# Performance work log

Measured on AMD Instinct MI355X. Metric: run time of the kernel, lower is better.

## Reference

```python
import jax, jax.numpy as jnp
import numpy as np

B, N, M, C, H = 2, 256, 512, 256, 8
Dh = C // H          # head dim = 32
F = 256              # frequency_embedding_size
MAX_PERIOD = 10000.0


def setup_inputs() -> dict:
    rng = jax.random.key(0)
    ks = jax.random.split(rng, 12)
    s = 0.02

    def w(k, shape):
        return jax.random.normal(k, shape, jnp.float32) * s

    inp = {
        "query": jax.random.normal(ks[0], (B, N, C), jnp.float32),
        "key": jax.random.normal(ks[1], (B, M, C), jnp.float32),
        "query_pos": jax.random.uniform(ks[2], (B, N, M), jnp.float32),
        # attention projections (torch Linear stores W as (out,in))
        "Wq": w(ks[3], (C, C)), "bq": jnp.zeros((C,), jnp.float32),
        "Wk": w(ks[4], (C, C)),
        "Wv": w(ks[5], (C, C)), "bv": jnp.zeros((C,), jnp.float32),
        "Wo": w(ks[6], (C, C)), "bo": jnp.zeros((C,), jnp.float32),
        # ScalarEmbedder MLP: Linear(F, C) -> SiLU -> Linear(C, C)
        "W1": w(ks[7], (C, F)), "b1": jnp.zeros((C,), jnp.float32),
        "W2": w(ks[8], (C, C)), "b2": jnp.zeros((C,), jnp.float32),
        "freqs": jnp.exp(-np.log(MAX_PERIOD) * jnp.arange(F // 2, dtype=jnp.float32) / (F // 2)),
    }
    return inp


def reference(query, key, query_pos, Wq, bq, Wk, Wv, bv, Wo, bo, W1, b1, W2, b2, freqs):
    scale = Dh ** (-0.5)
    # projections -> (B, H, N/M, Dh)
    q = (query @ Wq.T + bq).reshape(B, N, H, Dh).transpose(0, 2, 1, 3)
    k = (key @ Wk.T).reshape(B, M, H, Dh).transpose(0, 2, 1, 3)
    v = (key @ Wv.T + bv).reshape(B, M, H, Dh).transpose(0, 2, 1, 3)
    # scalar positional embedding per (n, m) pair
    t = query_pos.reshape(-1)                              # (B*N*M,)
    tf = t[:, None] * freqs                                # (B*N*M, F/2)
    emb = jnp.concatenate([jnp.cos(tf), jnp.sin(tf)], -1)  # (B*N*M, F)
    pe = jax.nn.silu(emb @ W1.T + b1) @ W2.T + b2          # (B*N*M, C)
    pe = pe.reshape(B, N, M, H, Dh).transpose(0, 3, 1, 2, 4)  # (B,H,N,M,Dh)
    # gated scores: (q[:,:,:,None] * pe) . k  ==  einsum over d
    attn = jnp.einsum('bhnd,bhnmd,bhmd->bhnm', q, pe, k) * scale
    attn = jax.nn.softmax(attn, axis=-1)
    x = jnp.einsum('bhnm,bhmd->bhnd', attn, v)             # (B,H,N,Dh)
    x = x.transpose(0, 2, 1, 3).reshape(B, N, C)
    return x @ Wo.T + bo + query
```

## Files before the change

### kernel.cpp

```cpp
#include <hip/hip_runtime.h>

#define Bn 2
#define Nn 256
#define Mn 512
#define Cn 256
#define Hn 8
#define MT 64
#define SCALE_ 0.17677669529663687f

typedef short bf16x8 __attribute__((ext_vector_type(8)));
typedef short bf16x4 __attribute__((ext_vector_type(4)));
typedef float f32x4 __attribute__((ext_vector_type(4)));

static __device__ __forceinline__ float b2f(short s) {
    unsigned u = ((unsigned)(unsigned short)s) << 16;
    return __builtin_bit_cast(float, u);
}
static __device__ __forceinline__ short f2b(float f) {
    unsigned u = __builtin_bit_cast(unsigned, f);
    u += 0x7fffu + ((u >> 16) & 1u);
    return (short)(u >> 16);
}
static __device__ __forceinline__ void async16(const void* g, void* l) {
    __builtin_amdgcn_global_load_lds(
        (const __attribute__((address_space(1))) unsigned int*)g,
        (__attribute__((address_space(3))) unsigned int*)l, 16, 0, 0);
}
static __device__ __forceinline__ int taddr(int c, int mm) {
    return (c >> 3) * 1040 + (c & 7) * 128 + (((mm >> 3) ^ (c & 7)) << 4) + (mm & 7) * 2;
}

__global__ __launch_bounds__(256) void prep(
        const float* __restrict__ query, const float* __restrict__ key,
        const float* __restrict__ Wq, const float* __restrict__ bq,
        const float* __restrict__ Wk, const float* __restrict__ Wv,
        const float* __restrict__ bv, const float* __restrict__ W1,
        const float* __restrict__ W2, short* __restrict__ W1b,
        short* __restrict__ W2b, float* __restrict__ qp,
        short* __restrict__ kTb, short* __restrict__ vTb) {
    __shared__ float arow[32][Cn];
    const int bid = blockIdx.x;
    const int t = threadIdx.x;
    if (bid < 256) {
        const int i = bid * 256 + t;
        W1b[i] = f2b(W1[i]);
        W2b[i] = f2b(W2[i]);
        return;
    }
    int task, id;
    if (bid < 320)      { task = 0; id = bid - 256; }
    else if (bid < 448) { task = 1; id = bid - 320; }
    else                { task = 2; id = bid - 448; }
    const int r0 = (id >> 2) * 32;
    const int c0 = (id & 3) * 64;
    const float* A = (task == 0) ? query : key;
    const float* W = (task == 0) ? Wq : (task == 1 ? Wk : Wv);
    #pragma unroll
    for (int i = 0; i < 32; ++i) arow[i][t] = A[(size_t)(r0 + i) * Cn + t];
    __syncthreads();
    const int col = c0 + (t & 63);
    const int rg = (t >> 6) * 8;
    float acc[8];
    #pragma unroll
    for (int i = 0; i < 8; ++i) acc[i] = 0.f;
    const float* wr = W + (size_t)col * Cn;
    for (int k = 0; k < Cn; k += 4) {
        const float4 wv = *(const float4*)(wr + k);
        #pragma unroll
        for (int i = 0; i < 8; ++i)
            acc[i] += arow[rg + i][k] * wv.x + arow[rg + i][k+1] * wv.y
                    + arow[rg + i][k+2] * wv.z + arow[rg + i][k+3] * wv.w;
    }
    if (task == 0) {
        const float bvv = bq[col];
        #pragma unroll
        for (int i = 0; i < 8; ++i)
            qp[(size_t)(r0 + rg + i) * Cn + col] = acc[i] + bvv;
    } else {
        const float bvv = (task == 2) ? bv[col] : 0.f;
        short* outb = (task == 2) ? vTb : kTb;
        const int b = r0 >> 9, mloc = (r0 & 511) + rg;
        bf16x8 p;
        #pragma unroll
        for (int i = 0; i < 8; ++i) p[i] = f2b(acc[i] + bvv);
        *(bf16x8*)(outb + ((size_t)(b * Cn + col)) * Mn + mloc) = p;
    }
}

__global__ __launch_bounds__(512)
__attribute__((amdgpu_waves_per_eu(2, 2)))
void fused_attn(
        const float* __restrict__ qp, const short* __restrict__ kTb,
        const short* __restrict__ vTb, const float* __restrict__ qpos,
        const short* __restrict__ W1b, const short* __restrict__ W2b,
        const float* __restrict__ b1, const float* __restrict__ b2,
        const float* __restrict__ freqs, float* __restrict__ xout) {
    __shared__ __align__(16) char embS[MT * 512];
    __shared__ __align__(16) char kTs[32 * 1040];
    __shared__ __align__(16) char vTs[32 * 1040];
    __shared__ float tposS[Mn];
    __shared__ float scb2[Hn * MT];
    __shared__ float pacc[512];
    __shared__ float corrS[Hn], lS[Hn];

    const int t = threadIdx.x;
    const int lane = t & 63;
    const int w = t >> 6;
    const int lr = lane & 15, lg = lane >> 4;

    const int qrow = ((blockIdx.x & 7) << 6) | (blockIdx.x >> 3);
    const int b = qrow >> 8;

    bf16x8 w1r[16], w2r[16];
    #pragma unroll
    for (int jb = 0; jb < 2; ++jb) {
        const short* p1 = W1b + (size_t)(w * 32 + jb * 16 + lr) * Cn + lg * 8;
        const short* p2 = W2b + (size_t)(w * 32 + jb * 16 + lr) * Cn + lg * 8;
        #pragma unroll
        for (int kk = 0; kk < 8; ++kk) {
            w1r[jb * 8 + kk] = *(const bf16x8*)(p1 + kk * 32);
            w2r[jb * 8 + kk] = *(const bf16x8*)(p2 + kk * 32);
        }
    }
    #pragma unroll
    for (int i = 0; i < 16; ++i) {
        asm volatile("" : "+v"(w1r[i]));
        asm volatile("" : "+v"(w2r[i]));
    }

    const int cA = w * 32 + lr, cB = cA + 16;
    const float b1v0 = b1[cA], b1v1 = b1[cB];
    const float b2v0 = b2[cA], b2v1 = b2[cB];
    const float q0 = qp[(size_t)qrow * Cn + cA];
    const float q1 = qp[(size_t)qrow * Cn + cB];
    const int fg = t & 7;
    float fr[16];
    #pragma unroll
    for (int j = 0; j < 16; ++j) fr[j] = freqs[fg * 16 + j];
    tposS[t] = qpos[(size_t)qrow * Mn + t];
    float m_run = -1e30f, l_run = 0.f;
    float xacc = 0.f;
    const f32x4 vzero = {0.f, 0.f, 0.f, 0.f};
    const int st_c = lane >> 3;
    const int st_ch = (lane & 7) ^ st_c;
    __syncthreads();

    for (int m0 = 0; m0 < Mn; m0 += MT) {
        {
            const size_t gb = (size_t)b * Cn * Mn + m0 + st_ch * 8;
            #pragma unroll
            for (int i = 0; i < 4; ++i) {
                const int seg = i * 8 + w;
                const size_t srow = gb + (size_t)(seg * 8 + st_c) * Mn;
                async16(kTb + srow, kTs + seg * 1040);
                async16(vTb + srow, vTs + seg * 1040);
            }
        }

        {
            const int m = t >> 3;
            const float tv = tposS[m0 + m];
            bf16x8 pc[2], ps[2];
            #pragma unroll
            for (int j = 0; j < 16; ++j) {
                float sv, cv;
                __sincosf(tv * fr[j], &sv, &cv);
                pc[j >> 3][j & 7] = f2b(cv);
                ps[j >> 3][j & 7] = f2b(sv);
            }
            char* rowp = embS + m * 512;
            const int sw = (m & 7) << 4;
            *(bf16x8*)(rowp + ((fg * 32) ^ sw)) = pc[0];
            *(bf16x8*)(rowp + ((fg * 32 + 16) ^ sw)) = pc[1];
            *(bf16x8*)(rowp + ((256 + fg * 32) ^ sw)) = ps[0];
            *(bf16x8*)(rowp + ((256 + fg * 32 + 16) ^ sw)) = ps[1];
        }
        __syncthreads();

        f32x4 acc[4][2];
        #pragma unroll
        for (int pb = 0; pb < 4; ++pb) { acc[pb][0] = vzero; acc[pb][1] = vzero; }
        #pragma unroll
        for (int pb = 0; pb < 4; ++pb) {
            const int row = pb * 16 + lr;
            const int sw = (row & 7) << 4;
            const char* rowp = embS + row * 512;
            #pragma unroll
            for (int kk = 0; kk < 8; ++kk) {
                const bf16x8 a = *(const bf16x8*)(rowp + ((lg * 16 + kk * 64) ^ sw));
                acc[pb][0] = __builtin_amdgcn_mfma_f32_16x16x32_bf16(a, w1r[kk],     acc[pb][0], 0, 0, 0);
                acc[pb][1] = __builtin_amdgcn_mfma_f32_16x16x32_bf16(a, w1r[8 + kk], acc[pb][1], 0, 0, 0);
            }
        }
        __syncthreads();

        #pragma unroll
        for (int pb = 0; pb < 4; ++pb) {
            #pragma unroll
            for (int jb = 0; jb < 2; ++jb) {
                const float bv = jb ? b1v1 : b1v0;
                const int j = w * 32 + jb * 16 + lr;
                #pragma unroll
                for (int r = 0; r < 4; ++r) {
                    const int row = pb * 16 + lg * 4 + r;
                    float hv = acc[pb][jb][r] + bv;
                    hv = hv / (1.f + __expf(-hv));
                    *(short*)(embS + row * 512 + ((j * 2) ^ ((row & 7) << 4))) = f2b(hv);
                }
            }
        }
        __syncthreads();

        #pragma unroll
        for (int pb = 0; pb < 4; ++pb) { acc[pb][0] = vzero; acc[pb][1] = vzero; }
        #pragma unroll
        for (int pb = 0; pb < 4; ++pb) {
            const int row = pb * 16 + lr;
            const int sw = (row & 7) << 4;
            const char* rowp = embS + row * 512;
            #pragma unroll
            for (int kk = 0; kk < 8; ++kk) {
                const bf16x8 a = *(const bf16x8*)(rowp + ((lg * 16 + kk * 64) ^ sw));
                acc[pb][0] = __builtin_amdgcn_mfma_f32_16x16x32_bf16(a, w2r[kk],     acc[pb][0], 0, 0, 0);
                acc[pb][1] = __builtin_amdgcn_mfma_f32_16x16x32_bf16(a, w2r[8 + kk], acc[pb][1], 0, 0, 0);
            }
        }

        #pragma unroll
        for (int pb = 0; pb < 4; ++pb) {
            const int mmb = pb * 16 + lg * 4;
            const bf16x4 k4a = *(const bf16x4*)(kTs + taddr(cA, mmb));
            const bf16x4 k4b = *(const bf16x4*)(kTs + taddr(cB, mmb));
            #pragma unroll
            for (int r = 0; r < 4; ++r) {
                float v = (acc[pb][0][r] + b2v0) * q0 * b2f(k4a[r])
                        + (acc[pb][1][r] + b2v1) * q1 * b2f(k4b[r]);
                v += __shfl_xor(v, 1);
                v += __shfl_xor(v, 2);
                v += __shfl_xor(v, 4);
                v += __shfl_xor(v, 8);
                if (lr == 0) scb2[w * MT + mmb + r] = v * SCALE_;
            }
        }

        {
            const float s = scb2[w * MT + lane];
            float tmax = s;
            #pragma unroll
            for (int msk = 1; msk < 64; msk <<= 1) tmax = fmaxf(tmax, __shfl_xor(tmax, msk));
            const float mnew = fmaxf(m_run, tmax);
            const float corr = __expf(m_run - mnew);
            const float e = __expf(s - mnew);
            scb2[w * MT + lane] = e;
            float ss = e;
            #pragma unroll
            for (int msk = 1; msk < 64; msk <<= 1) ss += __shfl_xor(ss, msk);
            l_run = l_run * corr + ss;
            m_run = mnew;
            if (lane == 0) corrS[w] = corr;
        }
        __syncthreads();

        {
            const int c = t & 255, half = t >> 8;
            const int h = c >> 5;
            const int rowb = (c >> 3) * 1040 + (c & 7) * 128;
            const int c7 = c & 7;
            const float* wr2 = scb2 + h * MT + half * 32;
            float s = 0.f;
            #pragma unroll
            for (int i = 0; i < 4; ++i) {
                const bf16x8 v8 = *(const bf16x8*)(vTs + rowb + (((half * 4 + i) ^ c7) << 4));
                const float4 wa = *(const float4*)(wr2 + i * 8);
                const float4 wb = *(const float4*)(wr2 + i * 8 + 4);
                s += wa.x * b2f(v8[0]) + wa.y * b2f(v8[1]) + wa.z * b2f(v8[2]) + wa.w * b2f(v8[3])
                   + wb.x * b2f(v8[4]) + wb.y * b2f(v8[5]) + wb.z * b2f(v8[6]) + wb.w * b2f(v8[7]);
            }
            pacc[t] = s;
        }
        __syncthreads();
        if (t < 256) xacc = xacc * corrS[t >> 5] + pacc[t] + pacc[t + 256];
    }

    if (lane == 0) lS[w] = l_run;
    __syncthreads();
    if (t < 256) xout[(size_t)qrow * Cn + t] = xacc / lS[t >> 5];
}

__global__ __launch_bounds__(256) void linear_out(
        const float* __restrict__ A, const float* __restrict__ W,
        const float* __restrict__ bias, const float* __restrict__ res,
        float* __restrict__ out) {
    __shared__ float arow[32][Cn];
    const int r0 = blockIdx.x * 32;
    const int c0 = blockIdx.y * 64;
    const int t = threadIdx.x;
    #pragma unroll
    for (int i = 0; i < 32; ++i) arow[i][t] = A[(size_t)(r0 + i) * Cn + t];
    __syncthreads();
    const int col = c0 + (t & 63);
    const int rg = (t >> 6) * 8;
    float acc[8];
    #pragma unroll
    for (int i = 0; i < 8; ++i) acc[i] = 0.f;
    const float* wr = W + (size_t)col * Cn;
    for (int k = 0; k < Cn; k += 4) {
        const float4 wv = *(const float4*)(wr + k);
        #pragma unroll
        for (int i = 0; i < 8; ++i)
            acc[i] += arow[rg + i][k] * wv.x + arow[rg + i][k+1] * wv.y
                    + arow[rg + i][k+2] * wv.z + arow[rg + i][k+3] * wv.w;
    }
    const float bvv = bias[col];
    #pragma unroll
    for (int i = 0; i < 8; ++i)
        out[(size_t)(r0 + rg + i) * Cn + col] =
            acc[i] + bvv + res[(size_t)(r0 + rg + i) * Cn + col];
}

extern "C" void kernel_launch(void* const* d_in, const int* in_sizes, int n_in,
                              void* d_out, int out_size, void* d_ws, size_t ws_size,
                              hipStream_t stream) {
    const float* query = (const float*)d_in[0];
    const float* key   = (const float*)d_in[1];
    const float* qpos  = (const float*)d_in[2];
    const float* Wq    = (const float*)d_in[3];
    const float* bq    = (const float*)d_in[4];
    const float* Wk    = (const float*)d_in[5];
    const float* Wv    = (const float*)d_in[6];
    const float* bv    = (const float*)d_in[7];
    const float* Wo    = (const float*)d_in[8];
    const float* bo    = (const float*)d_in[9];
    const float* W1    = (const float*)d_in[10];
    const float* b1    = (const float*)d_in[11];
    const float* W2    = (const float*)d_in[12];
    const float* b2    = (const float*)d_in[13];
    const float* freqs = (const float*)d_in[14];
    float* out = (float*)d_out;

    char* ws = (char*)d_ws;
    float* qp  = (float*)(ws);
    short* kTb = (short*)(ws + 524288);
    short* vTb = (short*)(ws + 1048576);
    float* xo  = (float*)(ws + 1572864);
    short* W1b = (short*)(ws + 2097152);
    short* W2b = (short*)(ws + 2228224);

    prep<<<576, 256, 0, stream>>>(query, key, Wq, bq, Wk, Wv, bv, W1, W2,
                                  W1b, W2b, qp, kTb, vTb);
    fused_attn<<<Bn * Nn, 512, 0, stream>>>(qp, kTb, vTb, qpos, W1b, W2b, b1, b2, freqs, xo);
    linear_out<<<dim3(16, 4), 256, 0, stream>>>(xo, Wo, bo, query, out);
}
```

Baseline: 299.8 us.

## Cut register and LDS use in fused attention, raise occupancy, re-grid projections

The fused attention kernel stops holding both W1 and W2 fragments in registers for the whole run. It keeps one shared register buffer and reloads W1 or W2 from global memory before each MLP stage. The async K/V staging into LDS is dropped, so K and V are read directly from global memory, and the launch bounds now request 4 blocks per CU. Sin/cos use hardware sinf/cosf on inputs pre-scaled by 1/2π. The prep and output-projection kernels are split into smaller tiles to launch more blocks. The trade-off is repeated weight and K/V global traffic and lower-precision trig in exchange for more waves in flight.

```diff
diff --git a/kernel.cpp b/kernel.cpp
--- a/kernel.cpp
+++ b/kernel.cpp
@@ -7,6 +7,7 @@
 #define Hn 8
 #define MT 64
 #define SCALE_ 0.17677669529663687f
+#define INV2PI 0.15915494309189535f
 
 typedef short bf16x8 __attribute__((ext_vector_type(8)));
 typedef short bf16x4 __attribute__((ext_vector_type(4)));
@@ -20,14 +21,6 @@
     unsigned u = __builtin_bit_cast(unsigned, f);
     u += 0x7fffu + ((u >> 16) & 1u);
     return (short)(u >> 16);
-}
-static __device__ __forceinline__ void async16(const void* g, void* l) {
-    __builtin_amdgcn_global_load_lds(
-        (const __attribute__((address_space(1))) unsigned int*)g,
-        (__attribute__((address_space(3))) unsigned int*)l, 16, 0, 0);
-}
-static __device__ __forceinline__ int taddr(int c, int mm) {
-    return (c >> 3) * 1040 + (c & 7) * 128 + (((mm >> 3) ^ (c & 7)) << 4) + (mm & 7) * 2;
 }
 
 __global__ __launch_bounds__(256) void prep(
@@ -47,58 +40,71 @@
         W2b[i] = f2b(W2[i]);
         return;
     }
-    int task, id;
-    if (bid < 320)      { task = 0; id = bid - 256; }
-    else if (bid < 448) { task = 1; id = bid - 320; }
-    else                { task = 2; id = bid - 448; }
-    const int r0 = (id >> 2) * 32;
-    const int c0 = (id & 3) * 64;
-    const float* A = (task == 0) ? query : key;
-    const float* W = (task == 0) ? Wq : (task == 1 ? Wk : Wv);
+    if (bid < 512) {
+        const int id = bid - 256;
+        const int r0 = (id >> 2) * 8, c0 = (id & 3) * 64;
+        #pragma unroll
+        for (int i = 0; i < 8; ++i)
+            if ((t >> 5) == i >> 2)
+                ;
+        #pragma unroll
+        for (int i = 0; i < 8; ++i) arow[i][t] = query[(size_t)(r0 + i) * Cn + t];
+        __syncthreads();
+        const int col = c0 + (t & 63);
+        const int rs = t >> 6;
+        float a0 = 0.f, a1 = 0.f;
+        const float* wr = Wq + (size_t)col * Cn;
+        for (int k = 0; k < Cn; k += 4) {
+            const float4 wv = *(const float4*)(wr + k);
+            const int r = rs * 2;
+            a0 += arow[r][k] * wv.x + arow[r][k+1] * wv.y
+                + arow[r][k+2] * wv.z + arow[r][k+3] * wv.w;
+            a1 += arow[r+1][k] * wv.x + arow[r+1][k+1] * wv.y
+                + arow[r+1][k+2] * wv.z + arow[r+1][k+3] * wv.w;
+        }
+        const float bvv = bq[col];
+        qp[(size_t)(r0 + rs * 2) * Cn + col] = a0 + bvv;
+        qp[(size_t)(r0 + rs * 2 + 1) * Cn + col] = a1 + bvv;
+        return;
+    }
+    const int isv = bid >= 768;
+    const int id = bid - (isv ? 768 : 512);
+    const int r0 = (id >> 3) * 32, c0 = (id & 7) * 32;
+    const float* W = isv ? Wv : Wk;
+    short* outb = isv ? vTb : kTb;
     #pragma unroll
-    for (int i = 0; i < 32; ++i) arow[i][t] = A[(size_t)(r0 + i) * Cn + t];
+    for (int i = 0; i < 32; ++i) arow[i][t] = key[(size_t)(r0 + i) * Cn + t];
     __syncthreads();
-    const int col = c0 + (t & 63);
-    const int rg = (t >> 6) * 8;
-    float acc[8];
-    #pragma unroll
-    for (int i = 0; i < 8; ++i) acc[i] = 0.f;
+    const int col = c0 + (t & 31);
+    const int rs = t >> 5;
+    float a4[4] = {0.f, 0.f, 0.f, 0.f};
     const float* wr = W + (size_t)col * Cn;
     for (int k = 0; k < Cn; k += 4) {
         const float4 wv = *(const float4*)(wr + k);
         #pragma unroll
-        for (int i = 0; i < 8; ++i)
-            acc[i] += arow[rg + i][k] * wv.x + arow[rg + i][k+1] * wv.y
-                    + arow[rg + i][k+2] * wv.z + arow[rg + i][k+3] * wv.w;
-    }
-    if (task == 0) {
-        const float bvv = bq[col];
-        #pragma unroll
-        for (int i = 0; i < 8; ++i)
-            qp[(size_t)(r0 + rg + i) * Cn + col] = acc[i] + bvv;
-    } else {
-        const float bvv = (task == 2) ? bv[col] : 0.f;
-        short* outb = (task == 2) ? vTb : kTb;
-        const int b = r0 >> 9, mloc = (r0 & 511) + rg;
-        bf16x8 p;
-        #pragma unroll
-        for (int i = 0; i < 8; ++i) p[i] = f2b(acc[i] + bvv);
-        *(bf16x8*)(outb + ((size_t)(b * Cn + col)) * Mn + mloc) = p;
-    }
-}
-
-__global__ __launch_bounds__(512)
-__attribute__((amdgpu_waves_per_eu(2, 2)))
-void fused_attn(
+        for (int i = 0; i < 4; ++i) {
+            const int r = rs * 4 + i;
+            a4[i] += arow[r][k] * wv.x + arow[r][k+1] * wv.y
+                   + arow[r][k+2] * wv.z + arow[r][k+3] * wv.w;
+        }
+    }
+    const float bvv = isv ? bv[col] : 0.f;
+    const int bk = r0 >> 9, mloc = (r0 & 511) + rs * 4;
+    bf16x4 p;
+    #pragma unroll
+    for (int i = 0; i < 4; ++i) p[i] = f2b(a4[i] + bvv);
+    *(bf16x4*)(outb + (size_t)(bk * Cn + col) * Mn + mloc) = p;
+}
+
+__global__ __launch_bounds__(512, 4) void fused_attn(
         const float* __restrict__ qp, const short* __restrict__ kTb,
         const short* __restrict__ vTb, const float* __restrict__ qpos,
         const short* __restrict__ W1b, const short* __restrict__ W2b,
         const float* __restrict__ b1, const float* __restrict__ b2,
         const float* __restrict__ freqs, float* __restrict__ xout) {
     __shared__ __align__(16) char embS[MT * 512];
-    __shared__ __align__(16) char kTs[32 * 1040];
-    __shared__ __align__(16) char vTs[32 * 1040];
     __shared__ float tposS[Mn];
+    __shared__ float fbuf[128];
     __shared__ float scb2[Hn * MT];
     __shared__ float pacc[512];
     __shared__ float corrS[Hn], lS[Hn];
@@ -111,62 +117,42 @@
     const int qrow = ((blockIdx.x & 7) << 6) | (blockIdx.x >> 3);
     const int b = qrow >> 8;
 
-    bf16x8 w1r[16], w2r[16];
+    const int cA = w * 32 + lr, cB = cA + 16;
+    const short* w1p0 = W1b + (size_t)cA * Cn + lg * 8;
+    const short* w1p1 = W1b + (size_t)cB * Cn + lg * 8;
+    const short* w2p0 = W2b + (size_t)cA * Cn + lg * 8;
+    const short* w2p1 = W2b + (size_t)cB * Cn + lg * 8;
+
+    bf16x8 wreg[16];
     #pragma unroll
-    for (int jb = 0; jb < 2; ++jb) {
-        const short* p1 = W1b + (size_t)(w * 32 + jb * 16 + lr) * Cn + lg * 8;
-        const short* p2 = W2b + (size_t)(w * 32 + jb * 16 + lr) * Cn + lg * 8;
-        #pragma unroll
-        for (int kk = 0; kk < 8; ++kk) {
-            w1r[jb * 8 + kk] = *(const bf16x8*)(p1 + kk * 32);
-            w2r[jb * 8 + kk] = *(const bf16x8*)(p2 + kk * 32);
-        }
-    }
-    #pragma unroll
-    for (int i = 0; i < 16; ++i) {
-        asm volatile("" : "+v"(w1r[i]));
-        asm volatile("" : "+v"(w2r[i]));
-    }
-
-    const int cA = w * 32 + lr, cB = cA + 16;
+    for (int kk = 0; kk < 8; ++kk) {
+        wreg[kk] = *(const bf16x8*)(w1p0 + kk * 32);
+        wreg[8 + kk] = *(const bf16x8*)(w1p1 + kk * 32);
+    }
+
     const float b1v0 = b1[cA], b1v1 = b1[cB];
     const float b2v0 = b2[cA], b2v1 = b2[cB];
     const float q0 = qp[(size_t)qrow * Cn + cA];
     const float q1 = qp[(size_t)qrow * Cn + cB];
-    const int fg = t & 7;
-    float fr[16];
-    #pragma unroll
-    for (int j = 0; j < 16; ++j) fr[j] = freqs[fg * 16 + j];
     tposS[t] = qpos[(size_t)qrow * Mn + t];
+    if (t < 128) fbuf[t] = freqs[t] * INV2PI;
+    const short* krow0 = kTb + (size_t)(b * Cn + cA) * Mn;
+    const short* krow1 = kTb + (size_t)(b * Cn + cB) * Mn;
     float m_run = -1e30f, l_run = 0.f;
     float xacc = 0.f;
     const f32x4 vzero = {0.f, 0.f, 0.f, 0.f};
-    const int st_c = lane >> 3;
-    const int st_ch = (lane & 7) ^ st_c;
     __syncthreads();
 
     for (int m0 = 0; m0 < Mn; m0 += MT) {
         {
-            const size_t gb = (size_t)b * Cn * Mn + m0 + st_ch * 8;
-            #pragma unroll
-            for (int i = 0; i < 4; ++i) {
-                const int seg = i * 8 + w;
-                const size_t srow = gb + (size_t)(seg * 8 + st_c) * Mn;
-                async16(kTb + srow, kTs + seg * 1040);
-                async16(vTb + srow, vTs + seg * 1040);
-            }
-        }
-
-        {
-            const int m = t >> 3;
+            const int m = t >> 3, fg = t & 7;
             const float tv = tposS[m0 + m];
             bf16x8 pc[2], ps[2];
             #pragma unroll
             for (int j = 0; j < 16; ++j) {
-                float sv, cv;
-                __sincosf(tv * fr[j], &sv, &cv);
-                pc[j >> 3][j & 7] = f2b(cv);
-                ps[j >> 3][j & 7] = f2b(sv);
+                const float xr = tv * fbuf[fg * 16 + j];
+                pc[j >> 3][j & 7] = f2b(__builtin_amdgcn_cosf(xr));
+                ps[j >> 3][j & 7] = f2b(__builtin_amdgcn_sinf(xr));
             }
             char* rowp = embS + m * 512;
             const int sw = (m & 7) << 4;
@@ -188,9 +174,14 @@
             #pragma unroll
             for (int kk = 0; kk < 8; ++kk) {
                 const bf16x8 a = *(const bf16x8*)(rowp + ((lg * 16 + kk * 64) ^ sw));
-                acc[pb][0] = __builtin_amdgcn_mfma_f32_16x16x32_bf16(a, w1r[kk],     acc[pb][0], 0, 0, 0);
-                acc[pb][1] = __builtin_amdgcn_mfma_f32_16x16x32_bf16(a, w1r[8 + kk], acc[pb][1], 0, 0, 0);
-            }
+                acc[pb][0] = __builtin_amdgcn_mfma_f32_16x16x32_bf16(a, wreg[kk],     acc[pb][0], 0, 0, 0);
+                acc[pb][1] = __builtin_amdgcn_mfma_f32_16x16x32_bf16(a, wreg[8 + kk], acc[pb][1], 0, 0, 0);
+            }
+        }
+        #pragma unroll
+        for (int kk = 0; kk < 8; ++kk) {
+            wreg[kk] = *(const bf16x8*)(w2p0 + kk * 32);
+            wreg[8 + kk] = *(const bf16x8*)(w2p1 + kk * 32);
         }
         __syncthreads();
 
@@ -221,16 +212,21 @@
             #pragma unroll
             for (int kk = 0; kk < 8; ++kk) {
                 const bf16x8 a = *(const bf16x8*)(rowp + ((lg * 16 + kk * 64) ^ sw));
-                acc[pb][0] = __builtin_amdgcn_mfma_f32_16x16x32_bf16(a, w2r[kk],     acc[pb][0], 0, 0, 0);
-                acc[pb][1] = __builtin_amdgcn_mfma_f32_16x16x32_bf16(a, w2r[8 + kk], acc[pb][1], 0, 0, 0);
-            }
+                acc[pb][0] = __builtin_amdgcn_mfma_f32_16x16x32_bf16(a, wreg[kk],     acc[pb][0], 0, 0, 0);
+                acc[pb][1] = __builtin_amdgcn_mfma_f32_16x16x32_bf16(a, wreg[8 + kk], acc[pb][1], 0, 0, 0);
+            }
+        }
+        #pragma unroll
+        for (int kk = 0; kk < 8; ++kk) {
+            wreg[kk] = *(const bf16x8*)(w1p0 + kk * 32);
+            wreg[8 + kk] = *(const bf16x8*)(w1p1 + kk * 32);
         }
 
         #pragma unroll
         for (int pb = 0; pb < 4; ++pb) {
             const int mmb = pb * 16 + lg * 4;
-            const bf16x4 k4a = *(const bf16x4*)(kTs + taddr(cA, mmb));
-            const bf16x4 k4b = *(const bf16x4*)(kTs + taddr(cB, mmb));
+            const bf16x4 k4a = *(const bf16x4*)(krow0 + m0 + mmb);
+            const bf16x4 k4b = *(const bf16x4*)(krow1 + m0 + mmb);
             #pragma unroll
             for (int r = 0; r < 4; ++r) {
                 float v = (acc[pb][0][r] + b2v0) * q0 * b2f(k4a[r])
@@ -264,13 +260,12 @@
         {
             const int c = t & 255, half = t >> 8;
             const int h = c >> 5;
-            const int rowb = (c >> 3) * 1040 + (c & 7) * 128;
-            const int c7 = c & 7;
+            const short* vrow = vTb + (size_t)(b * Cn + c) * Mn + m0 + half * 32;
             const float* wr2 = scb2 + h * MT + half * 32;
             float s = 0.f;
             #pragma unroll
             for (int i = 0; i < 4; ++i) {
-                const bf16x8 v8 = *(const bf16x8*)(vTs + rowb + (((half * 4 + i) ^ c7) << 4));
+                const bf16x8 v8 = *(const bf16x8*)(vrow + i * 8);
                 const float4 wa = *(const float4*)(wr2 + i * 8);
                 const float4 wb = *(const float4*)(wr2 + i * 8 + 4);
                 s += wa.x * b2f(v8[0]) + wa.y * b2f(v8[1]) + wa.z * b2f(v8[2]) + wa.w * b2f(v8[3])
@@ -291,31 +286,29 @@
         const float* __restrict__ A, const float* __restrict__ W,
         const float* __restrict__ bias, const float* __restrict__ res,
         float* __restrict__ out) {
-    __shared__ float arow[32][Cn];
-    const int r0 = blockIdx.x * 32;
+    __shared__ float arow[8][Cn];
+    const int r0 = blockIdx.x * 8;
     const int c0 = blockIdx.y * 64;
     const int t = threadIdx.x;
     #pragma unroll
-    for (int i = 0; i < 32; ++i) arow[i][t] = A[(size_t)(r0 + i) * Cn + t];
+    for (int i = 0; i < 8; ++i) arow[i][t] = A[(size_t)(r0 + i) * Cn + t];
     __syncthreads();
     const int col = c0 + (t & 63);
-    const int rg = (t >> 6) * 8;
-    float acc[8];
-    #pragma unroll
-    for (int i = 0; i < 8; ++i) acc[i] = 0.f;
+    const int rs = t >> 6;
+    float a0 = 0.f, a1 = 0.f;
     const float* wr = W + (size_t)col * Cn;
     for (int k = 0; k < Cn; k += 4) {
         const float4 wv = *(const float4*)(wr + k);
-        #pragma unroll
-        for (int i = 0; i < 8; ++i)
-            acc[i] += arow[rg + i][k] * wv.x + arow[rg + i][k+1] * wv.y
-                    + arow[rg + i][k+2] * wv.z + arow[rg + i][k+3] * wv.w;
+        const int r = rs * 2;
+        a0 += arow[r][k] * wv.x + arow[r][k+1] * wv.y
+            + arow[r][k+2] * wv.z + arow[r][k+3] * wv.w;
+        a1 += arow[r+1][k] * wv.x + arow[r+1][k+1] * wv.y
+            + arow[r+1][k+2] * wv.z + arow[r+1][k+3] * wv.w;
     }
     const float bvv = bias[col];
-    #pragma unroll
-    for (int i = 0; i < 8; ++i)
-        out[(size_t)(r0 + rg + i) * Cn + col] =
-            acc[i] + bvv + res[(size_t)(r0 + rg + i) * Cn + col];
+    const int row0 = r0 + rs * 2;
+    out[(size_t)row0 * Cn + col] = a0 + bvv + res[(size_t)row0 * Cn + col];
+    out[(size_t)(row0 + 1) * Cn + col] = a1 + bvv + res[(size_t)(row0 + 1) * Cn + col];
 }
 
 extern "C" void kernel_launch(void* const* d_in, const int* in_sizes, int n_in,
@@ -346,8 +339,8 @@
     short* W1b = (short*)(ws + 2097152);
     short* W2b = (short*)(ws + 2228224);
 
-    prep<<<576, 256, 0, stream>>>(query, key, Wq, bq, Wk, Wv, bv, W1, W2,
-                                  W1b, W2b, qp, kTb, vTb);
+    prep<<<1024, 256, 0, stream>>>(query, key, Wq, bq, Wk, Wv, bv, W1, W2,
+                                   W1b, W2b, qp, kTb, vTb);
     fused_attn<<<Bn * Nn, 512, 0, stream>>>(qp, kTb, vTb, qpos, W1b, W2b, b1, b2, freqs, xo);
-    linear_out<<<dim3(16, 4), 256, 0, stream>>>(xo, Wo, bo, query, out);
-}
+    linear_out<<<dim3(64, 4), 256, 0, stream>>>(xo, Wo, bo, query, out);
+}
```

Result: slower. 440.4 us (+46.9%).
